# Kernel optimization log

Measured on AMD Instinct MI355X. Metric: run time of the kernel, lower is better.

Reference implementation:

```python
import jax, jax.numpy as jnp
import numpy as np

B = 65536
D_IN = 8
H1, H2 = 256, 256


def setup_inputs() -> dict:
    key = jax.random.key(0)
    ks = jax.random.split(key, 12)
    def lin(kw, kb, fan_in, fan_out):
        s = 1.0 / np.sqrt(fan_in)
        W = jax.random.uniform(kw, (fan_out, fan_in), jnp.float32, -s, s)
        b = jax.random.uniform(kb, (fan_out,), jnp.float32, -s, s)
        return W, b
    W0, b0 = lin(ks[0], ks[1], D_IN, H1)
    W1, b1 = lin(ks[2], ks[3], H1, H2)
    W2, b2 = lin(ks[4], ks[5], H2, 1)
    W3, b3 = lin(ks[6], ks[7], 1, 8)
    x_batch = jax.random.normal(ks[8], (B, D_IN), jnp.float32)
    scores_x_batch = jax.random.normal(ks[9], (B, D_IN), jnp.float32)
    c = jnp.zeros((), jnp.float32)  # init_val parameter
    return {"x_batch": x_batch, "scores_x_batch": scores_x_batch,
            "W0": W0, "b0": b0, "W1": W1, "b1": b1,
            "W2": W2, "b2": b2, "W3": W3, "b3": b3, "c": c}


def reference(x_batch, scores_x_batch, W0, b0, W1, b1, W2, b2, W3, b3, c):
    # singleforwardpass: tanh on all layers except the last
    def single(x):  # x: [8] -> [8]
        y = jnp.tanh(W0 @ x + b0)
        y = jnp.tanh(W1 @ y + b1)
        y = jnp.tanh(W2 @ y + b2)
        return W3 @ y + b3

    eye = jnp.eye(D_IN, dtype=x_batch.dtype)

    def per_sample(x, score):
        # jacobian(single, x).diag().sum() + dot(single(x), score) + c
        u, lin_fn = jax.linearize(single, x)
        J = jax.vmap(lin_fn)(eye)        # [8, 8] (columns of Jacobian as rows)
        div = jnp.trace(J)               # sum of Jacobian diagonal
        return c + div + jnp.dot(u, score)

    return jax.vmap(per_sample)(x_batch, scores_x_batch)  # [B]
```

## Files before the change

### kernel.cpp

```cpp
#include <hip/hip_runtime.h>
#include <hip/hip_bf16.h>

#define B_TOTAL 65536
#define H 256
#define TS 64
#define THREADS 512
#define STRIDE 264

typedef __attribute__((ext_vector_type(8))) short bf16x8;
typedef __attribute__((ext_vector_type(4))) float f32x4;

__device__ __forceinline__ void tanh_r(float x, float& t, float& r) {
    float e = __expf(x + x);
    r = __builtin_amdgcn_rcpf(e + 1.0f);
    t = fmaf(-2.0f, r, 1.0f);
}
__device__ __forceinline__ float bf2f(ushort b) {
    union { unsigned u; float f; } v; v.u = ((unsigned)b) << 16;
    return v.f;
}
__device__ __forceinline__ ushort f2bf(float f) {
    union { float f; unsigned u; } v; v.f = f;
    unsigned r = v.u + 0x7fffu + ((v.u >> 16) & 1u);
    return (ushort)(r >> 16);
}
__device__ __forceinline__ ushort2 cvt2(float a, float b) {
    union { __hip_bfloat162 h; ushort2 u; } v;
    v.h = __float22bfloat162_rn(make_float2(a, b));
    return v.u;
}
__device__ __forceinline__ bf16x8 pack8(float4 a, float4 b) {
    union { bf16x8 v; ushort2 u[4]; } r;
    r.u[0] = cvt2(a.x, a.y); r.u[1] = cvt2(a.z, a.w);
    r.u[2] = cvt2(b.x, b.y); r.u[3] = cvt2(b.z, b.w);
    return r.v;
}

__global__ void pack_weights(const float* __restrict__ W1, ushort* __restrict__ pack) {
    int g = blockIdx.x * 256 + threadIdx.x;
    int jt = g >> 9;
    int ks = (g >> 6) & 7;
    int l  = g & 63;
    int row = jt * 16 + (l & 15);
    int k0  = ks * 32 + (l >> 4) * 8;
    ushort* dst = pack + (size_t)g * 8;
    const float* src = W1 + (size_t)row * H + k0;
#pragma unroll
    for (int t = 0; t < 8; ++t) dst[t] = f2bf(src[t]);
}

__launch_bounds__(THREADS, 4)
__global__ void fused_mlp(const float* __restrict__ x_batch,
                          const float* __restrict__ scores,
                          const float* __restrict__ W0, const float* __restrict__ b0,
                          const float* __restrict__ b1,
                          const float* __restrict__ W2, const float* __restrict__ b2,
                          const float* __restrict__ W3, const float* __restrict__ b3,
                          const float* __restrict__ cptr,
                          const ushort* __restrict__ packs,
                          float* __restrict__ out) {
    __shared__ ushort Y0[TS][STRIDE];
    __shared__ ushort DG[TS][STRIDE];
    __shared__ float  G0[H];
    __shared__ float  Z2p[4][TS];
    __shared__ float  Trp[4][TS];

    const int tid  = threadIdx.x;
    const int lane = tid & 63;
    const int w    = tid >> 6;
    const int bs   = blockIdx.x * TS;
    const int cl   = lane & 15;
    const int q    = lane >> 4;
    const int rq   = q * 4;
    const int j0   = w * 32;
    const int wj   = w & 3;
    const int sb   = (w >> 2) * 32;

    const ushort* pW = packs + (size_t)(4 * wj) * 4096 + (size_t)lane * 8;

    if (tid < H) {
        const float* wr = W0 + (size_t)tid * 8;
        float4 wa = *(const float4*)wr, wb = *(const float4*)(wr + 4);
        float4 w3a = *(const float4*)W3, w3b = *(const float4*)(W3 + 4);
        G0[tid] = wa.x * w3a.x + wa.y * w3a.y + wa.z * w3a.z + wa.w * w3a.w
                + wb.x * w3b.x + wb.y * w3b.y + wb.z * w3b.z + wb.w * w3b.w;
    }

    f32x4 l0[2][4];
    {
        bf16x8 bx[4];
#pragma unroll
        for (int st = 0; st < 4; ++st) {
            bf16x8 p = (bf16x8){0, 0, 0, 0, 0, 0, 0, 0};
            if (q == 0) {
                const float* xr = x_batch + (size_t)(bs + st * 16 + cl) * 8;
                p = pack8(*(const float4*)xr, *(const float4*)(xr + 4));
            }
            bx[st] = p;
        }
        const float* wr0 = W0 + (size_t)(j0 + cl) * 8;
        const float* wr1 = W0 + (size_t)(j0 + 16 + cl) * 8;
        bf16x8 af0 = pack8(*(const float4*)wr0, *(const float4*)(wr0 + 4));
        bf16x8 af1 = pack8(*(const float4*)wr1, *(const float4*)(wr1 + 4));
#pragma unroll
        for (int st = 0; st < 4; ++st) {
            f32x4 z = (f32x4){0.f, 0.f, 0.f, 0.f};
            l0[0][st] = __builtin_amdgcn_mfma_f32_16x16x32_bf16(af0, bx[st], z, 0, 0, 0);
            l0[1][st] = __builtin_amdgcn_mfma_f32_16x16x32_bf16(af1, bx[st], z, 0, 0, 0);
        }
    }
    __syncthreads();

    {
        float4 b0v0 = *(const float4*)(b0 + j0 + rq);
        float4 b0v1 = *(const float4*)(b0 + j0 + 16 + rq);
        float4 g0v0 = *(const float4*)&G0[j0 + rq];
        float4 g0v1 = *(const float4*)&G0[j0 + 16 + rq];
#pragma unroll
        for (int st = 0; st < 4; ++st) {
            const int row = st * 16 + cl;
#pragma unroll
            for (int jt = 0; jt < 2; ++jt) {
                f32x4 z = l0[jt][st];
                float4 bv = jt ? b0v1 : b0v0;
                float4 gv = jt ? g0v1 : g0v0;
                float t0, t1, t2, t3, r0, r1, r2, r3;
                tanh_r(z[0] + bv.x, t0, r0); tanh_r(z[1] + bv.y, t1, r1);
                tanh_r(z[2] + bv.z, t2, r2); tanh_r(z[3] + bv.w, t3, r3);
                ushort2 lo = cvt2(t0, t1), hi = cvt2(t2, t3);
                ushort4 vv; vv.x = lo.x; vv.y = lo.y; vv.z = hi.x; vv.w = hi.y;
                *(ushort4*)&Y0[row][j0 + jt * 16 + rq] = vv;
                float m0 = 4.f * r0, m1 = 4.f * r1, m2 = 4.f * r2, m3 = 4.f * r3;
                float d0 = fmaf(-m0, r0, m0), d1 = fmaf(-m1, r1, m1);
                float d2 = fmaf(-m2, r2, m2), d3 = fmaf(-m3, r3, m3);
                lo = cvt2(d0 * gv.x, d1 * gv.y); hi = cvt2(d2 * gv.z, d3 * gv.w);
                vv.x = lo.x; vv.y = lo.y; vv.z = hi.x; vv.w = hi.y;
                *(ushort4*)&DG[row][j0 + jt * 16 + rq] = vv;
            }
        }
    }

    bf16x8 wf0_ = *(const bf16x8*)(pW);
    bf16x8 wf1_ = *(const bf16x8*)(pW + 4096);
    bf16x8 wf2_ = *(const bf16x8*)(pW + 8192);
    bf16x8 wf3_ = *(const bf16x8*)(pW + 12288);

    __syncthreads();

    f32x4 facc[4][2], bacc[4][2];
#pragma unroll
    for (int jj = 0; jj < 4; ++jj)
#pragma unroll
        for (int stl = 0; stl < 2; ++stl) {
            facc[jj][stl] = (f32x4){0.f, 0.f, 0.f, 0.f};
            bacc[jj][stl] = (f32x4){0.f, 0.f, 0.f, 0.f};
        }
#pragma unroll 1
    for (int ks = 0; ks < 8; ++ks) {
        bf16x8 wn0 = wf0_, wn1 = wf1_, wn2 = wf2_, wn3 = wf3_;
        if (ks < 7) {
            const ushort* pn = pW + (size_t)(ks + 1) * 512;
            wn0 = *(const bf16x8*)(pn);
            wn1 = *(const bf16x8*)(pn + 4096);
            wn2 = *(const bf16x8*)(pn + 8192);
            wn3 = *(const bf16x8*)(pn + 12288);
        }
        const int k0 = ks * 32 + q * 8;
#pragma unroll
        for (int stl = 0; stl < 2; ++stl) {
            bf16x8 by = *(const bf16x8*)&Y0[sb + stl * 16 + cl][k0];
            bf16x8 bd = *(const bf16x8*)&DG[sb + stl * 16 + cl][k0];
            facc[0][stl] = __builtin_amdgcn_mfma_f32_16x16x32_bf16(wf0_, by, facc[0][stl], 0, 0, 0);
            bacc[0][stl] = __builtin_amdgcn_mfma_f32_16x16x32_bf16(wf0_, bd, bacc[0][stl], 0, 0, 0);
            facc[1][stl] = __builtin_amdgcn_mfma_f32_16x16x32_bf16(wf1_, by, facc[1][stl], 0, 0, 0);
            bacc[1][stl] = __builtin_amdgcn_mfma_f32_16x16x32_bf16(wf1_, bd, bacc[1][stl], 0, 0, 0);
            facc[2][stl] = __builtin_amdgcn_mfma_f32_16x16x32_bf16(wf2_, by, facc[2][stl], 0, 0, 0);
            bacc[2][stl] = __builtin_amdgcn_mfma_f32_16x16x32_bf16(wf2_, bd, bacc[2][stl], 0, 0, 0);
            facc[3][stl] = __builtin_amdgcn_mfma_f32_16x16x32_bf16(wf3_, by, facc[3][stl], 0, 0, 0);
            bacc[3][stl] = __builtin_amdgcn_mfma_f32_16x16x32_bf16(wf3_, bd, bacc[3][stl], 0, 0, 0);
        }
        wf0_ = wn0; wf1_ = wn1; wf2_ = wn2; wf3_ = wn3;
    }

    {
        float4 b1v[4], w2v[4];
#pragma unroll
        for (int jj = 0; jj < 4; ++jj) {
            b1v[jj] = *(const float4*)(b1 + wj * 64 + jj * 16 + rq);
            w2v[jj] = *(const float4*)(W2 + wj * 64 + jj * 16 + rq);
        }
#pragma unroll
        for (int stl = 0; stl < 2; ++stl) {
            float zp = 0.f, tp = 0.f;
#pragma unroll
            for (int jj = 0; jj < 4; ++jj) {
                f32x4 z  = facc[jj][stl];
                f32x4 mm = bacc[jj][stl];
                float4 bv = b1v[jj];
                float4 wv = w2v[jj];
                float t0, t1, t2, t3, r0, r1, r2, r3;
                tanh_r(z[0] + bv.x, t0, r0); tanh_r(z[1] + bv.y, t1, r1);
                tanh_r(z[2] + bv.z, t2, r2); tanh_r(z[3] + bv.w, t3, r3);
                zp = fmaf(wv.x, t0, zp); zp = fmaf(wv.y, t1, zp);
                zp = fmaf(wv.z, t2, zp); zp = fmaf(wv.w, t3, zp);
                float m0 = 4.f * wv.x * r0, m1 = 4.f * wv.y * r1;
                float m2 = 4.f * wv.z * r2, m3 = 4.f * wv.w * r3;
                float a0 = fmaf(-m0, r0, m0), a1 = fmaf(-m1, r1, m1);
                float a2 = fmaf(-m2, r2, m2), a3 = fmaf(-m3, r3, m3);
                tp = fmaf(a0, mm[0], tp); tp = fmaf(a1, mm[1], tp);
                tp = fmaf(a2, mm[2], tp); tp = fmaf(a3, mm[3], tp);
            }
            zp += __shfl_xor(zp, 16);
            zp += __shfl_xor(zp, 32);
            tp += __shfl_xor(tp, 16);
            tp += __shfl_xor(tp, 32);
            if (lane < 16) {
                Z2p[wj][sb + stl * 16 + lane] = zp;
                Trp[wj][sb + stl * 16 + lane] = tp;
            }
        }
    }
    __syncthreads();

    if (tid < TS) {
        const int s = tid;
        float z2 = b2[0], tr = 0.f;
#pragma unroll
        for (int k = 0; k < 4; ++k) { z2 += Z2p[k][s]; tr += Trp[k][s]; }
        float y2, r2;
        tanh_r(z2, y2, r2);
        float m2 = 4.0f * r2;
        float dy2 = fmaf(-m2, r2, m2);
        float4 w3a = *(const float4*)W3;
        float4 w3b = *(const float4*)(W3 + 4);
        float4 b3a = *(const float4*)b3;
        float4 b3b = *(const float4*)(b3 + 4);
        const float* sc = scores + (size_t)(bs + s) * 8;
        float4 s0 = *(const float4*)sc;
        float4 s1 = *(const float4*)(sc + 4);
        float p1 = w3a.x * s0.x + w3a.y * s0.y + w3a.z * s0.z + w3a.w * s0.w
                 + w3b.x * s1.x + w3b.y * s1.y + w3b.z * s1.z + w3b.w * s1.w;
        float p2 = b3a.x * s0.x + b3a.y * s0.y + b3a.z * s0.z + b3a.w * s0.w
                 + b3b.x * s1.x + b3b.y * s1.y + b3b.z * s1.z + b3b.w * s1.w;
        out[bs + s] = cptr[0] + dy2 * tr + fmaf(y2, p1, p2);
    }
}

extern "C" void kernel_launch(void* const* d_in, const int* in_sizes, int n_in,
                              void* d_out, int out_size, void* d_ws, size_t ws_size,
                              hipStream_t stream) {
    const float* x  = (const float*)d_in[0];
    const float* sc = (const float*)d_in[1];
    const float* W0 = (const float*)d_in[2];
    const float* b0 = (const float*)d_in[3];
    const float* W1 = (const float*)d_in[4];
    const float* b1 = (const float*)d_in[5];
    const float* W2 = (const float*)d_in[6];
    const float* b2 = (const float*)d_in[7];
    const float* W3 = (const float*)d_in[8];
    const float* b3 = (const float*)d_in[9];
    const float* c  = (const float*)d_in[10];
    float* out = (float*)d_out;
    ushort* packs = (ushort*)d_ws;

    hipLaunchKernelGGL(pack_weights, dim3(32), dim3(256), 0, stream, W1, packs);
    hipLaunchKernelGGL(fused_mlp, dim3(B_TOTAL / TS), dim3(THREADS), 0, stream,
                       x, sc, W0, b0, b1, W2, b2, W3, b3, c, packs, out);
}
```

Baseline: 35.05 us.

## Drop separate W1 packing kernel and convert fp32 weights to bf16 inline

Removes the pack_weights pre-kernel and its workspace. Each wave now loads W1 rows directly from fp32 global memory and converts them to bf16 MFMA fragments inside a fully unrolled k-loop. This saves a kernel launch and the dependency between the two kernels. In exchange, every block reads twice the weight bytes (fp32 instead of bf16) and repeats the conversion work, and the prefetch double-buffering is gone, which adds register pressure and may expose global load latency.

After: 73.54 us. +109.8%, slower.

```diff
diff --git a/kernel.cpp b/kernel.cpp
--- a/kernel.cpp
+++ b/kernel.cpp
@@ -19,11 +19,6 @@
     union { unsigned u; float f; } v; v.u = ((unsigned)b) << 16;
     return v.f;
 }
-__device__ __forceinline__ ushort f2bf(float f) {
-    union { float f; unsigned u; } v; v.f = f;
-    unsigned r = v.u + 0x7fffu + ((v.u >> 16) & 1u);
-    return (ushort)(r >> 16);
-}
 __device__ __forceinline__ ushort2 cvt2(float a, float b) {
     union { __hip_bfloat162 h; ushort2 u; } v;
     v.h = __float22bfloat162_rn(make_float2(a, b));
@@ -36,28 +31,14 @@
     return r.v;
 }
 
-__global__ void pack_weights(const float* __restrict__ W1, ushort* __restrict__ pack) {
-    int g = blockIdx.x * 256 + threadIdx.x;
-    int jt = g >> 9;
-    int ks = (g >> 6) & 7;
-    int l  = g & 63;
-    int row = jt * 16 + (l & 15);
-    int k0  = ks * 32 + (l >> 4) * 8;
-    ushort* dst = pack + (size_t)g * 8;
-    const float* src = W1 + (size_t)row * H + k0;
-#pragma unroll
-    for (int t = 0; t < 8; ++t) dst[t] = f2bf(src[t]);
-}
-
 __launch_bounds__(THREADS, 4)
 __global__ void fused_mlp(const float* __restrict__ x_batch,
                           const float* __restrict__ scores,
                           const float* __restrict__ W0, const float* __restrict__ b0,
-                          const float* __restrict__ b1,
+                          const float* __restrict__ W1, const float* __restrict__ b1,
                           const float* __restrict__ W2, const float* __restrict__ b2,
                           const float* __restrict__ W3, const float* __restrict__ b3,
                           const float* __restrict__ cptr,
-                          const ushort* __restrict__ packs,
                           float* __restrict__ out) {
     __shared__ ushort Y0[TS][STRIDE];
     __shared__ ushort DG[TS][STRIDE];
@@ -75,8 +56,6 @@
     const int j0   = w * 32;
     const int wj   = w & 3;
     const int sb   = (w >> 2) * 32;
-
-    const ushort* pW = packs + (size_t)(4 * wj) * 4096 + (size_t)lane * 8;
 
     if (tid < H) {
         const float* wr = W0 + (size_t)tid * 8;
@@ -139,12 +118,6 @@
             }
         }
     }
-
-    bf16x8 wf0_ = *(const bf16x8*)(pW);
-    bf16x8 wf1_ = *(const bf16x8*)(pW + 4096);
-    bf16x8 wf2_ = *(const bf16x8*)(pW + 8192);
-    bf16x8 wf3_ = *(const bf16x8*)(pW + 12288);
-
     __syncthreads();
 
     f32x4 facc[4][2], bacc[4][2];
@@ -155,31 +128,28 @@
             facc[jj][stl] = (f32x4){0.f, 0.f, 0.f, 0.f};
             bacc[jj][stl] = (f32x4){0.f, 0.f, 0.f, 0.f};
         }
-#pragma unroll 1
+#pragma unroll
     for (int ks = 0; ks < 8; ++ks) {
-        bf16x8 wn0 = wf0_, wn1 = wf1_, wn2 = wf2_, wn3 = wf3_;
-        if (ks < 7) {
-            const ushort* pn = pW + (size_t)(ks + 1) * 512;
-            wn0 = *(const bf16x8*)(pn);
-            wn1 = *(const bf16x8*)(pn + 4096);
-            wn2 = *(const bf16x8*)(pn + 8192);
-            wn3 = *(const bf16x8*)(pn + 12288);
-        }
         const int k0 = ks * 32 + q * 8;
+        bf16x8 wf[4];
+#pragma unroll
+        for (int jj = 0; jj < 4; ++jj) {
+            const float* wr = W1 + (size_t)(wj * 64 + jj * 16 + cl) * H + k0;
+            wf[jj] = pack8(*(const float4*)wr, *(const float4*)(wr + 4));
+        }
 #pragma unroll
         for (int stl = 0; stl < 2; ++stl) {
             bf16x8 by = *(const bf16x8*)&Y0[sb + stl * 16 + cl][k0];
             bf16x8 bd = *(const bf16x8*)&DG[sb + stl * 16 + cl][k0];
-            facc[0][stl] = __builtin_amdgcn_mfma_f32_16x16x32_bf16(wf0_, by, facc[0][stl], 0, 0, 0);
-            bacc[0][stl] = __builtin_amdgcn_mfma_f32_16x16x32_bf16(wf0_, bd, bacc[0][stl], 0, 0, 0);
-            facc[1][stl] = __builtin_amdgcn_mfma_f32_16x16x32_bf16(wf1_, by, facc[1][stl], 0, 0, 0);
-            bacc[1][stl] = __builtin_amdgcn_mfma_f32_16x16x32_bf16(wf1_, bd, bacc[1][stl], 0, 0, 0);
-            facc[2][stl] = __builtin_amdgcn_mfma_f32_16x16x32_bf16(wf2_, by, facc[2][stl], 0, 0, 0);
-            bacc[2][stl] = __builtin_amdgcn_mfma_f32_16x16x32_bf16(wf2_, bd, bacc[2][stl], 0, 0, 0);
-            facc[3][stl] = __builtin_amdgcn_mfma_f32_16x16x32_bf16(wf3_, by, facc[3][stl], 0, 0, 0);
-            bacc[3][stl] = __builtin_amdgcn_mfma_f32_16x16x32_bf16(wf3_, bd, bacc[3][stl], 0, 0, 0);
-        }
-        wf0_ = wn0; wf1_ = wn1; wf2_ = wn2; wf3_ = wn3;
+            facc[0][stl] = __builtin_amdgcn_mfma_f32_16x16x32_bf16(wf[0], by, facc[0][stl], 0, 0, 0);
+            bacc[0][stl] = __builtin_amdgcn_mfma_f32_16x16x32_bf16(wf[0], bd, bacc[0][stl], 0, 0, 0);
+            facc[1][stl] = __builtin_amdgcn_mfma_f32_16x16x32_bf16(wf[1], by, facc[1][stl], 0, 0, 0);
+            bacc[1][stl] = __builtin_amdgcn_mfma_f32_16x16x32_bf16(wf[1], bd, bacc[1][stl], 0, 0, 0);
+            facc[2][stl] = __builtin_amdgcn_mfma_f32_16x16x32_bf16(wf[2], by, facc[2][stl], 0, 0, 0);
+            bacc[2][stl] = __builtin_amdgcn_mfma_f32_16x16x32_bf16(wf[2], bd, bacc[2][stl], 0, 0, 0);
+            facc[3][stl] = __builtin_amdgcn_mfma_f32_16x16x32_bf16(wf[3], by, facc[3][stl], 0, 0, 0);
+            bacc[3][stl] = __builtin_amdgcn_mfma_f32_16x16x32_bf16(wf[3], bd, bacc[3][stl], 0, 0, 0);
+        }
     }
 
     {
@@ -261,9 +231,7 @@
     const float* b3 = (const float*)d_in[9];
     const float* c  = (const float*)d_in[10];
     float* out = (float*)d_out;
-    ushort* packs = (ushort*)d_ws;
-
-    hipLaunchKernelGGL(pack_weights, dim3(32), dim3(256), 0, stream, W1, packs);
+
     hipLaunchKernelGGL(fused_mlp, dim3(B_TOTAL / TS), dim3(THREADS), 0, stream,
-                       x, sc, W0, b0, b1, W2, b2, W3, b3, c, packs, out);
-}
+                       x, sc, W0, b0, W1, b1, W2, b2, W3, b3, c, out);
+}
```
